# Kernel tuning notes

Measured on AMD Instinct MI355X. Metric: run time of the kernel, lower is better.

The kernel has to match this reference:

```python
import jax, jax.numpy as jnp
import numpy as np

B, H, W, DIM, HEADS, WS, SHIFT, MLP_RATIO = 32, 56, 56, 256, 8, 7, 3, 4
N = WS * WS                      # tokens per window = 49
NW = (H // WS) * (W // WS)       # windows per image = 64
HEAD_DIM = DIM // HEADS
HIDDEN = DIM * MLP_RATIO


def _rel_index():
    # standard Swin relative position index, shape (N, N), values in [0, (2*WS-1)^2)
    coords = np.stack(np.meshgrid(np.arange(WS), np.arange(WS), indexing='ij')).reshape(2, -1)
    rel = (coords[:, :, None] - coords[:, None, :]).transpose(1, 2, 0)
    rel[:, :, 0] += WS - 1
    rel[:, :, 1] += WS - 1
    rel[:, :, 0] *= 2 * WS - 1
    return rel.sum(-1).astype(np.int32)


def _attn_mask():
    # shifted-window attention mask, shape (NW, N, N), values in {0, -100}
    img = np.zeros((H, W))
    slices = (slice(0, -WS), slice(-WS, -SHIFT), slice(-SHIFT, None))
    cnt = 0
    for hs in slices:
        for ws_ in slices:
            img[hs, ws_] = cnt
            cnt += 1
    mw = img.reshape(H // WS, WS, W // WS, WS).transpose(0, 2, 1, 3).reshape(-1, N)
    diff = mw[:, None, :] - mw[:, :, None]
    return np.where(diff != 0, -100.0, 0.0).astype(np.float32)


def setup_inputs() -> dict:
    key = jax.random.key(0)
    ks = jax.random.split(key, 16)
    s = 0.02
    return {
        'x': jax.random.normal(ks[0], (B, H * W, DIM), jnp.float32),
        'norm1_w': jnp.ones((DIM,), jnp.float32),
        'norm1_b': jnp.zeros((DIM,), jnp.float32),
        'qkv_w': jax.random.normal(ks[1], (3 * DIM, DIM), jnp.float32) * s,
        'qkv_b': jnp.zeros((3 * DIM,), jnp.float32),
        'rpb_table': jax.random.normal(ks[2], ((2 * WS - 1) ** 2, HEADS), jnp.float32) * s,
        'proj_w': jax.random.normal(ks[3], (DIM, DIM), jnp.float32) * s,
        'proj_b': jnp.zeros((DIM,), jnp.float32),
        'norm2_w': jnp.ones((DIM,), jnp.float32),
        'norm2_b': jnp.zeros((DIM,), jnp.float32),
        'fc1_w': jax.random.normal(ks[4], (HIDDEN, DIM), jnp.float32) * s,
        'fc1_b': jnp.zeros((HIDDEN,), jnp.float32),
        'fc2_w': jax.random.normal(ks[5], (DIM, HIDDEN), jnp.float32) * s,
        'fc2_b': jnp.zeros((DIM,), jnp.float32),
        'rel_idx': jnp.asarray(_rel_index()),
        'attn_mask': jnp.asarray(_attn_mask()),
    }


def _ln(t, w, b):
    mu = t.mean(-1, keepdims=True)
    var = ((t - mu) ** 2).mean(-1, keepdims=True)
    return (t - mu) * jax.lax.rsqrt(var + 1e-5) * w + b


def reference(x, norm1_w, norm1_b, qkv_w, qkv_b, rpb_table, proj_w, proj_b,
              norm2_w, norm2_b, fc1_w, fc1_b, fc2_w, fc2_b, rel_idx, attn_mask):
    Bz = x.shape[0]
    shortcut = x
    h = _ln(x, norm1_w, norm1_b).reshape(Bz, H, W, DIM)
    h = jnp.roll(h, (-SHIFT, -SHIFT), axis=(1, 2))                      # cyclic shift
    # window partition -> (Bz*NW, N, C)
    h = h.reshape(Bz, H // WS, WS, W // WS, WS, DIM).transpose(0, 1, 3, 2, 4, 5).reshape(-1, N, DIM)
    qkv = (h @ qkv_w.T + qkv_b).reshape(-1, N, 3, HEADS, HEAD_DIM).transpose(2, 0, 3, 1, 4)
    q, k, v = qkv[0], qkv[1], qkv[2]                                    # (Bz*NW, heads, N, d)
    scale = HEAD_DIM ** -0.5
    attn = jnp.einsum('whnd,whmd->whnm', q * scale, k)
    bias = rpb_table[rel_idx].transpose(2, 0, 1)                        # (heads, N, N)
    attn = attn + bias[None]
    attn = attn.reshape(Bz, NW, HEADS, N, N) + attn_mask[None, :, None]  # shift mask
    attn = jax.nn.softmax(attn.reshape(-1, HEADS, N, N), axis=-1)
    out = jnp.einsum('whnm,whmd->whnd', attn, v).transpose(0, 2, 1, 3).reshape(-1, N, DIM)
    out = out @ proj_w.T + proj_b
    # window reverse + un-shift
    out = out.reshape(Bz, H // WS, W // WS, WS, WS, DIM).transpose(0, 1, 3, 2, 4, 5).reshape(Bz, H, W, DIM)
    out = jnp.roll(out, (SHIFT, SHIFT), axis=(1, 2)).reshape(Bz, H * W, DIM)
    x = shortcut + out
    # residual MLP (pre-LN), exact GELU as in nn.GELU default
    h2 = _ln(x, norm2_w, norm2_b)
    h2 = jax.nn.gelu(h2 @ fc1_w.T + fc1_b, approximate=False)
    return x + (h2 @ fc2_w.T + fc2_b)
```

## Files before the change

### kernel.cpp

```cpp
#include <hip/hip_runtime.h>

typedef unsigned short ushort_t;
typedef __bf16 bf16_t;
typedef __attribute__((ext_vector_type(8))) __bf16 bf16x8;
typedef __attribute__((ext_vector_type(4))) float floatx4;

#define TOKS 100352

__device__ __forceinline__ ushort_t f2bf(float f) {
    union { float f; unsigned u; } a; a.f = f;
    unsigned r = a.u + 0x7fffu + ((a.u >> 16) & 1u);
    return (ushort_t)(r >> 16);
}

__device__ __forceinline__ void async16(const void* g, void* l) {
    __builtin_amdgcn_global_load_lds(
        (const __attribute__((address_space(1))) unsigned int*)g,
        (__attribute__((address_space(3))) unsigned int*)l,
        16, 0, 0);
}

__device__ __forceinline__ int win_to_orig(int t) {
    int b = t / 3136, rr = t - b * 3136;
    int w_ = rr / 49, pos = rr - w_ * 49;
    int wi = w_ >> 3, wj = w_ & 7;
    int ti = pos / 7, tj = pos - ti * 7;
    int h = wi * 7 + ti + 3; if (h >= 56) h -= 56;
    int w = wj * 7 + tj + 3; if (w >= 56) w -= 56;
    return b * 3136 + h * 56 + w;
}

__global__ void convert_kernel(const float* __restrict__ qkv_w, const float* __restrict__ proj_w,
                               const float* __restrict__ fc1_w, const float* __restrict__ fc2_w,
                               const float* __restrict__ rpb, const int* __restrict__ rel_idx,
                               ushort_t* __restrict__ wq, ushort_t* __restrict__ wp,
                               ushort_t* __restrict__ w1, ushort_t* __restrict__ w2,
                               float* __restrict__ bias_h) {
    int i = blockIdx.x * 256 + threadIdx.x;
    if (i < 196608) wq[i] = f2bf(qkv_w[i]);
    if (i < 65536)  wp[i] = f2bf(proj_w[i]);
    if (i < 262144) { w1[i] = f2bf(fc1_w[i]); w2[i] = f2bf(fc2_w[i]); }
    if (i < 19208)  {
        int h = i / 2401, ij = i - h * 2401;
        bias_h[i] = rpb[rel_idx[ij] * 8 + h];
    }
}

template <int GATHER>
__global__ __launch_bounds__(256) void ln_kernel(const float* __restrict__ xin,
                                                 const float* __restrict__ gw,
                                                 const float* __restrict__ gb,
                                                 ushort_t* __restrict__ outb) {
    const int wid = threadIdx.x >> 6, lane = threadIdx.x & 63;
    const int t_out = blockIdx.x * 4 + wid;
    const int t_in = GATHER ? win_to_orig(t_out) : t_out;
    const float4* src = (const float4*)(xin + (long)t_in * 256);
    float4 v = src[lane];
    float s  = v.x + v.y + v.z + v.w;
    float s2 = v.x*v.x + v.y*v.y + v.z*v.z + v.w*v.w;
    #pragma unroll
    for (int d = 32; d >= 1; d >>= 1) { s += __shfl_xor(s, d, 64); s2 += __shfl_xor(s2, d, 64); }
    float mu  = s * 0.00390625f;
    float var = s2 * 0.00390625f - mu * mu;
    float ry  = rsqrtf(var + 1e-5f);
    float4 w4 = ((const float4*)gw)[lane], b4 = ((const float4*)gb)[lane];
    unsigned long long p =
          (unsigned long long)f2bf((v.x - mu) * ry * w4.x + b4.x)
        | ((unsigned long long)f2bf((v.y - mu) * ry * w4.y + b4.y) << 16)
        | ((unsigned long long)f2bf((v.z - mu) * ry * w4.z + b4.z) << 32)
        | ((unsigned long long)f2bf((v.w - mu) * ry * w4.w + b4.w) << 48);
    ((unsigned long long*)(outb + (long)t_out * 256))[lane] = p;
}

template <int MODE, int N_LD, int KD>
__global__ __launch_bounds__(256, 2) void gemm_kernel(const ushort_t* __restrict__ A,
                                                      const ushort_t* __restrict__ Bw,
                                                      const float* __restrict__ bias,
                                                      void* __restrict__ outp,
                                                      const float* __restrict__ x_res) {
    __shared__ __align__(16) ushort_t As[128 * 32];
    __shared__ __align__(16) ushort_t Bs[128 * 32];
    const int tid = threadIdx.x;
    const int lane = tid & 63;
    const int wid = tid >> 6;
    const int wm = wid & 1, wn = wid >> 1;
    const int l15 = lane & 15, quad = lane >> 4;
    const long tileM = (long)blockIdx.y * 128;
    const long tileN = (long)blockIdx.x * 128;

    floatx4 acc[4][4];
    #pragma unroll
    for (int i = 0; i < 4; i++)
        #pragma unroll
        for (int j = 0; j < 4; j++) acc[i][j] = {0.f, 0.f, 0.f, 0.f};

    const int o1 = tid * 16;
    const int r1 = o1 >> 6, c1 = (o1 & 63) >> 1;
    const ushort_t* Ar1 = A + (tileM + r1) * KD + c1;
    const ushort_t* Ar2 = A + (tileM + r1 + 64) * KD + c1;
    const ushort_t* Br1 = Bw + (tileN + r1) * KD + c1;
    const ushort_t* Br2 = Bw + (tileN + r1 + 64) * KD + c1;
    ushort_t* Ad1 = &As[o1 >> 1];
    ushort_t* Ad2 = &As[(o1 >> 1) + 2048];
    ushort_t* Bd1 = &Bs[o1 >> 1];
    ushort_t* Bd2 = &Bs[(o1 >> 1) + 2048];

    for (int k0 = 0; k0 < KD; k0 += 32) {
        async16(Ar1 + k0, Ad1);
        async16(Ar2 + k0, Ad2);
        async16(Br1 + k0, Bd1);
        async16(Br2 + k0, Bd2);
        __syncthreads();
        bf16x8 af[4], bfr[4];
        #pragma unroll
        for (int mi = 0; mi < 4; mi++)
            af[mi] = *(const bf16x8*)&As[(wm * 64 + mi * 16 + l15) * 32 + quad * 8];
        #pragma unroll
        for (int nj = 0; nj < 4; nj++)
            bfr[nj] = *(const bf16x8*)&Bs[(wn * 64 + nj * 16 + l15) * 32 + quad * 8];
        #pragma unroll
        for (int mi = 0; mi < 4; mi++)
            #pragma unroll
            for (int nj = 0; nj < 4; nj++)
                acc[mi][nj] = __builtin_amdgcn_mfma_f32_16x16x32_bf16(af[mi], bfr[nj], acc[mi][nj], 0, 0, 0);
        __syncthreads();
    }

    #pragma unroll
    for (int mi = 0; mi < 4; mi++)
      #pragma unroll
      for (int nj = 0; nj < 4; nj++)
        #pragma unroll
        for (int r = 0; r < 4; r++) {
            long row = tileM + wm * 64 + mi * 16 + quad * 4 + r;
            long col = tileN + wn * 64 + nj * 16 + l15;
            float v = acc[mi][nj][r] + bias[col];
            if (MODE == 0) {
                ((ushort_t*)outp)[row * N_LD + col] = f2bf(v);
            } else if (MODE == 1) {
                int t_in = win_to_orig((int)row);
                long idx = (long)t_in * 256 + col;
                ((float*)outp)[idx] = v + x_res[idx];
            } else if (MODE == 2) {
                float g = 0.5f * v * (1.f + erff(v * 0.70710678118654752f));
                ((ushort_t*)outp)[row * N_LD + col] = f2bf(g);
            } else {
                ((float*)outp)[row * N_LD + col] += v;
            }
        }
}

__global__ __launch_bounds__(256, 2) void attn_kernel(const ushort_t* __restrict__ qkv,
                                                      const float* __restrict__ bias_h,
                                                      const float* __restrict__ mask,
                                                      ushort_t* __restrict__ attnout) {
    __shared__ __align__(16) ushort_t lds[4 * 6912];
    const int tid = threadIdx.x, lane = tid & 63, wid = tid >> 6;
    ushort_t* Pl = &lds[wid * 6912];
    ushort_t* Vt = Pl + 64 * 72;
    const int whid = blockIdx.x * 4 + wid;
    const int win = whid >> 3, head = whid & 7;
    const int wimg = win & 63;
    const int l15 = lane & 15, quad = lane >> 4;
    const long base = (long)win * 49 * 768;

    bf16x8 qf[4], kf[4];
    #pragma unroll
    for (int t4 = 0; t4 < 4; t4++) {
        int tok = t4 * 16 + l15; if (tok > 48) tok = 48;
        const ushort_t* p = qkv + base + (long)tok * 768 + head * 32 + quad * 8;
        qf[t4] = *(const bf16x8*)p;
        kf[t4] = *(const bf16x8*)(p + 256);
    }

    floatx4 S[4][4];
    #pragma unroll
    for (int mi = 0; mi < 4; mi++)
        #pragma unroll
        for (int nj = 0; nj < 4; nj++) {
            floatx4 z = {0.f, 0.f, 0.f, 0.f};
            S[mi][nj] = __builtin_amdgcn_mfma_f32_16x16x32_bf16(qf[mi], kf[nj], z, 0, 0, 0);
        }

    {
        int j = lane;
        int jc = j < 49 ? j : 48;
        const uint4* vsrc = (const uint4*)(qkv + base + (long)jc * 768 + 512 + head * 32);
        uint4 vz; vz.x = vz.y = vz.z = vz.w = 0u;
        #pragma unroll
        for (int q4 = 0; q4 < 4; q4++) {
            uint4 vv = (j < 49) ? vsrc[q4] : vz;
            int db = q4 * 8;
            Vt[(db+0)*72 + j] = (ushort_t)vv.x;  Vt[(db+1)*72 + j] = (ushort_t)(vv.x >> 16);
            Vt[(db+2)*72 + j] = (ushort_t)vv.y;  Vt[(db+3)*72 + j] = (ushort_t)(vv.y >> 16);
            Vt[(db+4)*72 + j] = (ushort_t)vv.z;  Vt[(db+5)*72 + j] = (ushort_t)(vv.z >> 16);
            Vt[(db+6)*72 + j] = (ushort_t)vv.w;  Vt[(db+7)*72 + j] = (ushort_t)(vv.w >> 16);
        }
    }

    const float scale = 0.17677669529663687f;
    const float* bh = bias_h + head * 2401;
    const float* mk = mask + wimg * 2401;
    #pragma unroll
    for (int mi = 0; mi < 4; mi++)
      #pragma unroll
      for (int nj = 0; nj < 4; nj++)
        #pragma unroll
        for (int r = 0; r < 4; r++) {
            int i = mi * 16 + quad * 4 + r;
            int j = nj * 16 + l15;
            float s = -1e30f;
            if (i < 49 && j < 49) {
                int ij = i * 49 + j;
                s = S[mi][nj][r] * scale + bh[ij] + mk[ij];
            }
            S[mi][nj][r] = s;
        }

    #pragma unroll
    for (int mi = 0; mi < 4; mi++)
      #pragma unroll
      for (int r = 0; r < 4; r++) {
          float m = fmaxf(fmaxf(S[mi][0][r], S[mi][1][r]), fmaxf(S[mi][2][r], S[mi][3][r]));
          #pragma unroll
          for (int d = 1; d < 16; d <<= 1) m = fmaxf(m, __shfl_xor(m, d, 64));
          float e[4], sum = 0.f;
          #pragma unroll
          for (int nj = 0; nj < 4; nj++) { e[nj] = __expf(S[mi][nj][r] - m); sum += e[nj]; }
          #pragma unroll
          for (int d = 1; d < 16; d <<= 1) sum += __shfl_xor(sum, d, 64);
          float rinv = 1.f / sum;
          int i = mi * 16 + quad * 4 + r;
          #pragma unroll
          for (int nj = 0; nj < 4; nj++) Pl[i * 72 + (nj * 16 + l15)] = f2bf(e[nj] * rinv);
      }

    __syncthreads();

    floatx4 O[4][2];
    #pragma unroll
    for (int mi = 0; mi < 4; mi++) { O[mi][0] = {0.f,0.f,0.f,0.f}; O[mi][1] = {0.f,0.f,0.f,0.f}; }
    #pragma unroll
    for (int kc = 0; kc < 2; kc++) {
        bf16x8 pf[4], vf[2];
        #pragma unroll
        for (int mi = 0; mi < 4; mi++)
            pf[mi] = *(const bf16x8*)&Pl[(mi * 16 + l15) * 72 + kc * 32 + quad * 8];
        #pragma unroll
        for (int n2 = 0; n2 < 2; n2++)
            vf[n2] = *(const bf16x8*)&Vt[(n2 * 16 + l15) * 72 + kc * 32 + quad * 8];
        #pragma unroll
        for (int mi = 0; mi < 4; mi++)
            #pragma unroll
            for (int n2 = 0; n2 < 2; n2++)
                O[mi][n2] = __builtin_amdgcn_mfma_f32_16x16x32_bf16(pf[mi], vf[n2], O[mi][n2], 0, 0, 0);
    }

    #pragma unroll
    for (int mi = 0; mi < 4; mi++)
      #pragma unroll
      for (int n2 = 0; n2 < 2; n2++)
        #pragma unroll
        for (int r = 0; r < 4; r++) {
            int i = mi * 16 + quad * 4 + r;
            if (i < 49) {
                long orow = ((long)win * 49 + i) * 256 + head * 32 + n2 * 16 + l15;
                attnout[orow] = f2bf(O[mi][n2][r]);
            }
        }
}

extern "C" void kernel_launch(void* const* d_in, const int* in_sizes, int n_in,
                              void* d_out, int out_size, void* d_ws, size_t ws_size,
                              hipStream_t stream) {
    const float* x      = (const float*)d_in[0];
    const float* n1w    = (const float*)d_in[1];
    const float* n1b    = (const float*)d_in[2];
    const float* qkv_w  = (const float*)d_in[3];
    const float* qkv_b  = (const float*)d_in[4];
    const float* rpb    = (const float*)d_in[5];
    const float* proj_w = (const float*)d_in[6];
    const float* proj_b = (const float*)d_in[7];
    const float* n2w    = (const float*)d_in[8];
    const float* n2b    = (const float*)d_in[9];
    const float* fc1_w  = (const float*)d_in[10];
    const float* fc1_b  = (const float*)d_in[11];
    const float* fc2_w  = (const float*)d_in[12];
    const float* fc2_b  = (const float*)d_in[13];
    const int*   rel_idx= (const int*)d_in[14];
    const float* amask  = (const float*)d_in[15];

    char* ws = (char*)d_ws;
    ushort_t* wq   = (ushort_t*)(ws + 0);
    ushort_t* wp   = (ushort_t*)(ws + 393216);
    ushort_t* w1   = (ushort_t*)(ws + 524288);
    ushort_t* w2   = (ushort_t*)(ws + 1048576);
    float*    bh   = (float*)   (ws + 1572864);
    ushort_t* hwin = (ushort_t*)(ws + 1703936);
    ushort_t* qkvb = (ushort_t*)(ws + 53084160);
    ushort_t* h2   = qkvb;
    ushort_t* h3   = (ushort_t*)(ws + 104464384);

    convert_kernel<<<1024, 256, 0, stream>>>(qkv_w, proj_w, fc1_w, fc2_w, rpb, rel_idx,
                                             wq, wp, w1, w2, bh);
    ln_kernel<1><<<TOKS / 4, 256, 0, stream>>>(x, n1w, n1b, hwin);
    gemm_kernel<0, 768, 256><<<dim3(6, 784), 256, 0, stream>>>(hwin, wq, qkv_b, qkvb, nullptr);
    attn_kernel<<<4096, 256, 0, stream>>>(qkvb, bh, amask, hwin);
    gemm_kernel<1, 256, 256><<<dim3(2, 784), 256, 0, stream>>>(hwin, wp, proj_b, d_out, x);
    ln_kernel<0><<<TOKS / 4, 256, 0, stream>>>((const float*)d_out, n2w, n2b, h2);
    for (int c = 0; c < 2; c++) {
        gemm_kernel<2, 1024, 256><<<dim3(8, 392), 256, 0, stream>>>(
            h2 + (long)c * 50176 * 256, w1, fc1_b, h3, nullptr);
        gemm_kernel<3, 256, 1024><<<dim3(2, 392), 256, 0, stream>>>(
            h3, w2, fc2_b, (float*)d_out + (long)c * 50176 * 256, nullptr);
    }
    (void)in_sizes; (void)n_in; (void)out_size; (void)ws_size;
}
```

Baseline: 700.7 us.

## Fuse proj GEMM with residual and LayerNorm, precombine bias and mask, defer softmax normalization

Replaces the separate projection GEMM and second LayerNorm kernel with one proj_ln_kernel. It computes a 64x256 output tile, adds the residual, writes x, and reduces row statistics across waves through LDS to emit the normalized bf16 tensor. This avoids re-reading x for the LN pass. The relative-position bias and shift mask are pre-summed into one per-window, per-head table staged in the output buffer, so attention needs one load instead of two. Attention now runs one wave per block and applies the softmax 1/sum after the PV product. The fused kernel launches only 1568 blocks and the combined bias table is about 4.9 MB, which adds extra traffic.

```diff
diff --git a/kernel.cpp b/kernel.cpp
--- a/kernel.cpp
+++ b/kernel.cpp
@@ -1,7 +1,6 @@
 #include <hip/hip_runtime.h>
 
 typedef unsigned short ushort_t;
-typedef __bf16 bf16_t;
 typedef __attribute__((ext_vector_type(8))) __bf16 bf16x8;
 typedef __attribute__((ext_vector_type(4))) float floatx4;
 
@@ -33,16 +32,18 @@
 __global__ void convert_kernel(const float* __restrict__ qkv_w, const float* __restrict__ proj_w,
                                const float* __restrict__ fc1_w, const float* __restrict__ fc2_w,
                                const float* __restrict__ rpb, const int* __restrict__ rel_idx,
+                               const float* __restrict__ amask,
                                ushort_t* __restrict__ wq, ushort_t* __restrict__ wp,
                                ushort_t* __restrict__ w1, ushort_t* __restrict__ w2,
-                               float* __restrict__ bias_h) {
+                               float* __restrict__ bm) {
     int i = blockIdx.x * 256 + threadIdx.x;
     if (i < 196608) wq[i] = f2bf(qkv_w[i]);
     if (i < 65536)  wp[i] = f2bf(proj_w[i]);
     if (i < 262144) { w1[i] = f2bf(fc1_w[i]); w2[i] = f2bf(fc2_w[i]); }
-    if (i < 19208)  {
-        int h = i / 2401, ij = i - h * 2401;
-        bias_h[i] = rpb[rel_idx[ij] * 8 + h];
+    if (i < 1229312) {
+        int wh = i / 2401, ij = i - wh * 2401;
+        int head = wh & 7, wimg = wh >> 3;
+        bm[i] = rpb[rel_idx[ij] * 8 + head] + amask[wimg * 2401 + ij];
     }
 }
 
@@ -76,8 +77,7 @@
 __global__ __launch_bounds__(256, 2) void gemm_kernel(const ushort_t* __restrict__ A,
                                                       const ushort_t* __restrict__ Bw,
                                                       const float* __restrict__ bias,
-                                                      void* __restrict__ outp,
-                                                      const float* __restrict__ x_res) {
+                                                      void* __restrict__ outp) {
     __shared__ __align__(16) ushort_t As[128 * 32];
     __shared__ __align__(16) ushort_t Bs[128 * 32];
     const int tid = threadIdx.x;
@@ -137,10 +137,6 @@
             float v = acc[mi][nj][r] + bias[col];
             if (MODE == 0) {
                 ((ushort_t*)outp)[row * N_LD + col] = f2bf(v);
-            } else if (MODE == 1) {
-                int t_in = win_to_orig((int)row);
-                long idx = (long)t_in * 256 + col;
-                ((float*)outp)[idx] = v + x_res[idx];
             } else if (MODE == 2) {
                 float g = 0.5f * v * (1.f + erff(v * 0.70710678118654752f));
                 ((ushort_t*)outp)[row * N_LD + col] = f2bf(g);
@@ -150,19 +146,106 @@
         }
 }
 
-__global__ __launch_bounds__(256, 2) void attn_kernel(const ushort_t* __restrict__ qkv,
-                                                      const float* __restrict__ bias_h,
-                                                      const float* __restrict__ mask,
-                                                      ushort_t* __restrict__ attnout) {
-    __shared__ __align__(16) ushort_t lds[4 * 6912];
+__global__ __launch_bounds__(256, 2) void proj_ln_kernel(
+        const ushort_t* __restrict__ A, const ushort_t* __restrict__ Bw,
+        const float* __restrict__ pb, const float* __restrict__ x_res,
+        const float* __restrict__ n2w, const float* __restrict__ n2b,
+        float* __restrict__ xout, ushort_t* __restrict__ h2out) {
+    __shared__ __align__(16) ushort_t As[64 * 32];
+    __shared__ __align__(16) ushort_t Bs[256 * 32];
+    __shared__ float red_s[4][64];
+    __shared__ float red_q[4][64];
     const int tid = threadIdx.x, lane = tid & 63, wid = tid >> 6;
-    ushort_t* Pl = &lds[wid * 6912];
-    ushort_t* Vt = Pl + 64 * 72;
-    const int whid = blockIdx.x * 4 + wid;
+    const int l15 = lane & 15, quad = lane >> 4;
+    const long tileM = (long)blockIdx.x * 64;
+
+    floatx4 acc[4][4];
+    #pragma unroll
+    for (int i = 0; i < 4; i++)
+        #pragma unroll
+        for (int j = 0; j < 4; j++) acc[i][j] = {0.f, 0.f, 0.f, 0.f};
+
+    const int oA = tid * 16;
+    const int rA = oA >> 6, cA = (oA & 63) >> 1;
+    const ushort_t* Ap = A + (tileM + rA) * 256 + cA;
+    ushort_t* Ad = &As[oA >> 1];
+
+    for (int k0 = 0; k0 < 256; k0 += 32) {
+        async16(Ap + k0, Ad);
+        #pragma unroll
+        for (int ch = 0; ch < 4; ch++) {
+            int o = ch * 4096 + oA;
+            async16(Bw + (o >> 6) * 256 + ((o & 63) >> 1) + k0, &Bs[o >> 1]);
+        }
+        __syncthreads();
+        bf16x8 af[4], bfr[4];
+        #pragma unroll
+        for (int mi = 0; mi < 4; mi++)
+            af[mi] = *(const bf16x8*)&As[(mi * 16 + l15) * 32 + quad * 8];
+        #pragma unroll
+        for (int nj = 0; nj < 4; nj++)
+            bfr[nj] = *(const bf16x8*)&Bs[(wid * 64 + nj * 16 + l15) * 32 + quad * 8];
+        #pragma unroll
+        for (int mi = 0; mi < 4; mi++)
+            #pragma unroll
+            for (int nj = 0; nj < 4; nj++)
+                acc[mi][nj] = __builtin_amdgcn_mfma_f32_16x16x32_bf16(af[mi], bfr[nj], acc[mi][nj], 0, 0, 0);
+        __syncthreads();
+    }
+
+    int orig[4][4];
+    #pragma unroll
+    for (int mi = 0; mi < 4; mi++)
+      #pragma unroll
+      for (int r = 0; r < 4; r++) {
+        int iloc = mi * 16 + quad * 4 + r;
+        orig[mi][r] = win_to_orig((int)tileM + iloc);
+        float s = 0.f, q = 0.f;
+        #pragma unroll
+        for (int nj = 0; nj < 4; nj++) {
+            int col = wid * 64 + nj * 16 + l15;
+            long gi = (long)orig[mi][r] * 256 + col;
+            float v = acc[mi][nj][r] + pb[col] + x_res[gi];
+            xout[gi] = v;
+            acc[mi][nj][r] = v;
+            s += v; q += v * v;
+        }
+        #pragma unroll
+        for (int d = 1; d < 16; d <<= 1) { s += __shfl_xor(s, d, 64); q += __shfl_xor(q, d, 64); }
+        if (l15 == 0) { red_s[wid][iloc] = s; red_q[wid][iloc] = q; }
+      }
+    __syncthreads();
+    #pragma unroll
+    for (int mi = 0; mi < 4; mi++)
+      #pragma unroll
+      for (int r = 0; r < 4; r++) {
+        int iloc = mi * 16 + quad * 4 + r;
+        float s = red_s[0][iloc] + red_s[1][iloc] + red_s[2][iloc] + red_s[3][iloc];
+        float q = red_q[0][iloc] + red_q[1][iloc] + red_q[2][iloc] + red_q[3][iloc];
+        float mu = s * 0.00390625f;
+        float var = q * 0.00390625f - mu * mu;
+        float rstd = rsqrtf(var + 1e-5f);
+        #pragma unroll
+        for (int nj = 0; nj < 4; nj++) {
+            int col = wid * 64 + nj * 16 + l15;
+            float v = acc[mi][nj][r];
+            h2out[(long)orig[mi][r] * 256 + col] = f2bf((v - mu) * rstd * n2w[col] + n2b[col]);
+        }
+      }
+}
+
+__global__ __launch_bounds__(64) void attn_kernel(const ushort_t* __restrict__ qkv,
+                                                  const float* __restrict__ bm,
+                                                  ushort_t* __restrict__ attnout) {
+    __shared__ __align__(16) ushort_t lds[96 * 72];
+    ushort_t* Pl = lds;
+    ushort_t* Vt = lds + 64 * 72;
+    const int lane = threadIdx.x;
+    const int whid = blockIdx.x;
     const int win = whid >> 3, head = whid & 7;
-    const int wimg = win & 63;
     const int l15 = lane & 15, quad = lane >> 4;
     const long base = (long)win * 49 * 768;
+    const float* bmw = bm + (long)((win & 63) * 8 + head) * 2401;
 
     bf16x8 qf[4], kf[4];
     #pragma unroll
@@ -199,8 +282,6 @@
     }
 
     const float scale = 0.17677669529663687f;
-    const float* bh = bias_h + head * 2401;
-    const float* mk = mask + wimg * 2401;
     #pragma unroll
     for (int mi = 0; mi < 4; mi++)
       #pragma unroll
@@ -210,13 +291,11 @@
             int i = mi * 16 + quad * 4 + r;
             int j = nj * 16 + l15;
             float s = -1e30f;
-            if (i < 49 && j < 49) {
-                int ij = i * 49 + j;
-                s = S[mi][nj][r] * scale + bh[ij] + mk[ij];
-            }
+            if (i < 49 && j < 49) s = S[mi][nj][r] * scale + bmw[i * 49 + j];
             S[mi][nj][r] = s;
         }
 
+    float rinv[4][4];
     #pragma unroll
     for (int mi = 0; mi < 4; mi++)
       #pragma unroll
@@ -229,10 +308,10 @@
           for (int nj = 0; nj < 4; nj++) { e[nj] = __expf(S[mi][nj][r] - m); sum += e[nj]; }
           #pragma unroll
           for (int d = 1; d < 16; d <<= 1) sum += __shfl_xor(sum, d, 64);
-          float rinv = 1.f / sum;
+          rinv[mi][r] = 1.f / sum;
           int i = mi * 16 + quad * 4 + r;
           #pragma unroll
-          for (int nj = 0; nj < 4; nj++) Pl[i * 72 + (nj * 16 + l15)] = f2bf(e[nj] * rinv);
+          for (int nj = 0; nj < 4; nj++) Pl[i * 72 + (nj * 16 + l15)] = f2bf(e[nj]);
       }
 
     __syncthreads();
@@ -265,7 +344,7 @@
             int i = mi * 16 + quad * 4 + r;
             if (i < 49) {
                 long orow = ((long)win * 49 + i) * 256 + head * 32 + n2 * 16 + l15;
-                attnout[orow] = f2bf(O[mi][n2][r]);
+                attnout[orow] = f2bf(O[mi][n2][r] * rinv[mi][r]);
             }
         }
 }
@@ -295,24 +374,23 @@
     ushort_t* wp   = (ushort_t*)(ws + 393216);
     ushort_t* w1   = (ushort_t*)(ws + 524288);
     ushort_t* w2   = (ushort_t*)(ws + 1048576);
-    float*    bh   = (float*)   (ws + 1572864);
-    ushort_t* hwin = (ushort_t*)(ws + 1703936);
-    ushort_t* qkvb = (ushort_t*)(ws + 53084160);
+    ushort_t* hwin = (ushort_t*)(ws + 1572864);
+    ushort_t* qkvb = (ushort_t*)(ws + 52953088);
     ushort_t* h2   = qkvb;
-    ushort_t* h3   = (ushort_t*)(ws + 104464384);
-
-    convert_kernel<<<1024, 256, 0, stream>>>(qkv_w, proj_w, fc1_w, fc2_w, rpb, rel_idx,
-                                             wq, wp, w1, w2, bh);
+    ushort_t* h3   = (ushort_t*)(ws + 104333312);
+    float* bm = (float*)d_out;
+
+    convert_kernel<<<4803, 256, 0, stream>>>(qkv_w, proj_w, fc1_w, fc2_w, rpb, rel_idx,
+                                             amask, wq, wp, w1, w2, bm);
     ln_kernel<1><<<TOKS / 4, 256, 0, stream>>>(x, n1w, n1b, hwin);
-    gemm_kernel<0, 768, 256><<<dim3(6, 784), 256, 0, stream>>>(hwin, wq, qkv_b, qkvb, nullptr);
-    attn_kernel<<<4096, 256, 0, stream>>>(qkvb, bh, amask, hwin);
-    gemm_kernel<1, 256, 256><<<dim3(2, 784), 256, 0, stream>>>(hwin, wp, proj_b, d_out, x);
-    ln_kernel<0><<<TOKS / 4, 256, 0, stream>>>((const float*)d_out, n2w, n2b, h2);
+    gemm_kernel<0, 768, 256><<<dim3(6, 784), 256, 0, stream>>>(hwin, wq, qkv_b, qkvb);
+    attn_kernel<<<16384, 64, 0, stream>>>(qkvb, bm, hwin);
+    proj_ln_kernel<<<1568, 256, 0, stream>>>(hwin, wp, proj_b, x, n2w, n2b, (float*)d_out, h2);
     for (int c = 0; c < 2; c++) {
         gemm_kernel<2, 1024, 256><<<dim3(8, 392), 256, 0, stream>>>(
-            h2 + (long)c * 50176 * 256, w1, fc1_b, h3, nullptr);
+            h2 + (long)c * 50176 * 256, w1, fc1_b, h3);
         gemm_kernel<3, 256, 1024><<<dim3(2, 392), 256, 0, stream>>>(
-            h3, w2, fc2_b, (float*)d_out + (long)c * 50176 * 256, nullptr);
+            h3, w2, fc2_b, (float*)d_out + (long)c * 50176 * 256);
     }
     (void)in_sizes; (void)n_in; (void)out_size; (void)ws_size;
 }
```

New measurement: 760.1 us. 1.08x slower.
